# Optimization experiments

Hardware: AMD Instinct MI355X
Metric: run time of the kernel (lower is better)

Reference implementation:

```python
import jax, jax.numpy as jnp
import numpy as np

TOPK = 8
N_EXPERTS = 64
ALPHA = 0.001


def setup_inputs() -> dict:
    key = jax.random.key(0)
    k1, k2 = jax.random.split(key)
    B, S, H = 4, 4096, 4096
    x = jax.random.normal(k1, (B, S, H), dtype=jnp.float32)
    # kaiming-uniform-ish router weight, bound = sqrt(6/((1+5)*H)) = 1/sqrt(H)
    bound = 1.0 / np.sqrt(H)
    weight = jax.random.uniform(k2, (N_EXPERTS, H), dtype=jnp.float32,
                                minval=-bound, maxval=bound)
    return {"x": x, "weight": weight}


def reference(x, weight):
    B, S, H = x.shape
    E = weight.shape[0]
    tokens = x.reshape(-1, H)                      # (T, H), T = B*S
    logits = jnp.einsum('th,eh->te', tokens, weight)  # router GEMM (T, E)
    scores = jax.nn.softmax(logits, axis=-1)
    # top-k selection (torch uses sorted=False; same set of values/indices)
    topk_weight, topk_idx = jax.lax.top_k(scores, TOPK)  # (T, k)
    # normalize top-k probs (norm_topk_prob=True, topk>1)
    topk_weight = topk_weight / (topk_weight.sum(axis=1, keepdims=True) + 1e-20)
    # seq-aux load-balancing loss (training path, alpha > 0, seq_aux=True)
    idx_flat = topk_idx.reshape(B, S * TOPK)                 # (B, S*k)
    ce = jax.nn.one_hot(idx_flat, E, dtype=jnp.float32).sum(axis=1)  # scatter_add of ones
    ce = ce / (S * TOPK / E)                                  # (B, E)
    mean_scores = scores.reshape(B, S, E).mean(axis=1)        # (B, E)
    aux_loss = (ce * mean_scores).sum(axis=1).mean() * ALPHA
    return topk_idx, topk_weight, aux_loss
```

## Files before the change

kernel.cpp:

```cpp
#include <hip/hip_runtime.h>
#include <math.h>

#define H 4096
#define NE 64
#define KTOP 8
#define BT 64
#define TTOT 16384
#define NBLK (TTOT / BT)
#define TAU 1e-4f
#define DELTA 1e-3f

typedef __attribute__((ext_vector_type(8))) short bf16x8;
typedef __attribute__((ext_vector_type(4))) float f32x4;

union U4S8 { uint4 u; bf16x8 s; };

__device__ __forceinline__ unsigned bf16_rne(float f) {
  unsigned b = __float_as_uint(f);
  b += 0x7fffu + ((b >> 16) & 1u);
  return b >> 16;
}

__global__ __launch_bounds__(256) void w_prep(const float* __restrict__ w,
                                              uint4* __restrict__ wsimg) {
  const int sid = blockIdx.x * 256 + threadIdx.x;
  const int e = sid >> 9;
  const int rem = sid & 511;
  const int c = rem >> 2;
  const int s = rem & 3;
  const float* src = w + (size_t)e * H + c * 32 + s * 8;
  float4 f0 = *(const float4*)src;
  float4 f1 = *(const float4*)(src + 4);
  float xf[8] = {f0.x, f0.y, f0.z, f0.w, f1.x, f1.y, f1.z, f1.w};
  unsigned hu[8], lu[8];
#pragma unroll
  for (int j = 0; j < 8; ++j) {
    hu[j] = bf16_rne(xf[j]);
    float hf = __uint_as_float(hu[j] << 16);
    lu[j] = bf16_rne(xf[j] - hf);
  }
  uint4 hp, lp;
  hp.x = hu[0] | (hu[1] << 16); hp.y = hu[2] | (hu[3] << 16);
  hp.z = hu[4] | (hu[5] << 16); hp.w = hu[6] | (hu[7] << 16);
  lp.x = lu[0] | (lu[1] << 16); lp.y = lu[2] | (lu[3] << 16);
  lp.z = lu[4] | (lu[5] << 16); lp.w = lu[6] | (lu[7] << 16);
  const int slotp = s ^ ((e >> 1) & 3);
  wsimg[(size_t)c * 256 + e * 4 + slotp] = hp;
  wsimg[(size_t)128 * 256 + (size_t)c * 256 + e * 4 + slotp] = lp;
}

__device__ __forceinline__ void cvt_split(const float4 a, const float4 b,
                                          bf16x8* hi, bf16x8* lo) {
  float xf[8] = {a.x, a.y, a.z, a.w, b.x, b.y, b.z, b.w};
  unsigned ph[4], pl[4];
#pragma unroll
  for (int q = 0; q < 4; ++q)
    asm("v_cvt_pk_bf16_f32 %0, %1, %2" : "=v"(ph[q])
        : "v"(xf[2 * q]), "v"(xf[2 * q + 1]));
  float rs[8];
#pragma unroll
  for (int q = 0; q < 4; ++q) {
    rs[2 * q]     = xf[2 * q]     - __uint_as_float(ph[q] << 16);
    rs[2 * q + 1] = xf[2 * q + 1] - __uint_as_float(ph[q] & 0xffff0000u);
  }
#pragma unroll
  for (int q = 0; q < 4; ++q)
    asm("v_cvt_pk_bf16_f32 %0, %1, %2" : "=v"(pl[q])
        : "v"(rs[2 * q]), "v"(rs[2 * q + 1]));
  U4S8 h, l;
  h.u = (uint4){ph[0], ph[1], ph[2], ph[3]};
  l.u = (uint4){pl[0], pl[1], pl[2], pl[3]};
  *hi = h.s;
  *lo = l.s;
}

#define GLDS(GP, LP)                                                   \
  __builtin_amdgcn_global_load_lds(                                    \
      (const __attribute__((address_space(1))) void*)(GP),             \
      (__attribute__((address_space(3))) void*)(LP), 16, 0, 0)

__global__ __launch_bounds__(256, 1) void moe_pass1(
    const float* __restrict__ x, const uint4* __restrict__ wsimg,
    float* __restrict__ out, unsigned* __restrict__ wmask,
    float* __restrict__ waux) {
  extern __shared__ __align__(16) char smraw[];
  const int tid = threadIdx.x;
  const int lane = tid & 63;
  const int wid = tid >> 6;
  const int tok0 = blockIdx.x * BT;
  const int trow = lane & 15;
  const int kgrp = lane >> 4;

  const char* xsrc[4];
#pragma unroll
  for (int j = 0; j < 4; ++j) {
    const int Lb = j * 4096 + tid * 16;
    const int row = Lb >> 8;
    const int inrow = Lb & 255;
    const int sin = inrow ^ ((row & 7) << 4);
    xsrc[j] = (const char*)(x + (size_t)(tok0 + row) * H) + sin;
  }
  const uint4* wsrc[4];
#pragma unroll
  for (int j = 0; j < 4; ++j)
    wsrc[j] = wsimg + (size_t)(j >> 1) * (128 * 256) + (j & 1) * 256 + tid;

  f32x4 acc[4];
#pragma unroll
  for (int et = 0; et < 4; ++et) acc[et] = (f32x4){0.f, 0.f, 0.f, 0.f};

#define ISSUE_STEP(KC, BUF)                                             \
  do {                                                                  \
    char* bb = smraw + (BUF) * 32768 + (wid << 10);                     \
    _Pragma("unroll") for (int j = 0; j < 4; ++j)                       \
      GLDS(xsrc[j] + (size_t)(KC) * 256, bb + j * 4096);                \
    _Pragma("unroll") for (int j = 0; j < 4; ++j)                       \
      GLDS((const char*)(wsrc[j] + (size_t)(KC) * 512),                 \
           bb + 16384 + j * 4096);                                      \
  } while (0)

  ISSUE_STEP(0, 0);
  ISSUE_STEP(1, 1);
  ISSUE_STEP(2, 2);

  const int arow = wid * 16 + trow;
  const int sx = (trow & 7) << 4;
  const int abase = arow * 256 + kgrp * 32;
  int entry[4];
#pragma unroll
  for (int et = 0; et < 4; ++et) {
    const int e = et * 16 + trow;
    entry[et] = (e * 4 + (kgrp ^ ((e >> 1) & 3))) * 16;
  }

#pragma unroll 1
  for (int kc = 0; kc < 64; ++kc) {
    if (kc < 62) {
      asm volatile("s_waitcnt vmcnt(16)" ::: "memory");
    } else if (kc == 62) {
      asm volatile("s_waitcnt vmcnt(8)" ::: "memory");
    } else {
      asm volatile("s_waitcnt vmcnt(0)" ::: "memory");
    }
    __builtin_amdgcn_s_barrier();
    asm volatile("" ::: "memory");
    if (kc + 3 < 64) ISSUE_STEP(kc + 3, (kc + 3) & 3);

    const char* bufp = smraw + (kc & 3) * 32768;
#pragma unroll
    for (int sub = 0; sub < 2; ++sub) {
      float4 v0 = *(const float4*)(bufp + ((abase + sub * 128) ^ sx));
      float4 v1 = *(const float4*)(bufp + ((abase + sub * 128 + 16) ^ sx));
      bf16x8 ah, al;
      cvt_split(v0, v1, &ah, &al);
#pragma unroll
      for (int et = 0; et < 4; ++et) {
        U4S8 bh, bl;
        bh.u = *(const uint4*)(bufp + 16384 + sub * 4096 + entry[et]);
        bl.u = *(const uint4*)(bufp + 16384 + (2 + sub) * 4096 + entry[et]);
        acc[et] = __builtin_amdgcn_mfma_f32_16x16x32_bf16(ah, bh.s, acc[et], 0, 0, 0);
        acc[et] = __builtin_amdgcn_mfma_f32_16x16x32_bf16(ah, bl.s, acc[et], 0, 0, 0);
        acc[et] = __builtin_amdgcn_mfma_f32_16x16x32_bf16(al, bh.s, acc[et], 0, 0, 0);
      }
    }
  }

  __syncthreads();
  float* lg = (float*)smraw;
  float* msumA = (float*)(smraw + 16896);
  float* cntA = (float*)(smraw + 17920);
#pragma unroll
  for (int et = 0; et < 4; ++et)
#pragma unroll
    for (int r = 0; r < 4; ++r)
      lg[(wid * 16 + kgrp * 4 + r) * 66 + et * 16 + trow] = acc[et][r];
  __syncthreads();

  float msum = 0.f;
  int cnt = 0;
#pragma unroll 1
  for (int it = 0; it < 16; ++it) {
    const int t = wid * 16 + it;
    const float lf = lg[t * 66 + lane];

    float m = lf;
#pragma unroll
    for (int off = 32; off; off >>= 1) m = fmaxf(m, __shfl_xor(m, off));
    float p = expf(lf - m);
    float s = p;
#pragma unroll
    for (int off = 32; off; off >>= 1) s += __shfl_xor(s, off);
    msum += p / s;

    float cur = lf;
    float myv = 0.f;
    int myi = 0;
#pragma unroll
    for (int r = 0; r < 9; ++r) {
      float v = cur;
      int ix = lane;
#pragma unroll
      for (int off = 1; off < 64; off <<= 1) {
        float ov = __shfl_xor(v, off);
        int oi = __shfl_xor(ix, off);
        if (ov > v || (ov == v && oi < ix)) { v = ov; ix = oi; }
      }
      if (lane == r) { myv = v; myi = ix; }
      if (r < 8 && lane == ix) { cur = -INFINITY; ++cnt; }
    }

    const float m0 = __shfl(myv, 0);
    float e = expf(myv - m0);
    float sv = e;
    sv += __shfl_xor(sv, 1);
    sv += __shfl_xor(sv, 2);
    sv += __shfl_xor(sv, 4);
    const float wgtv = e / sv;
    const int tg = tok0 + t;
    if (lane < KTOP) {
      out[(size_t)tg * KTOP + lane] = (float)myi;
      out[(size_t)TTOT * KTOP + (size_t)tg * KTOP + lane] = wgtv;
    }

    const float nxt = __shfl(myv, (lane + 1) & 63);
    const bool gp = (lane < 8) && (myv - nxt < TAU);
    const unsigned long long anyg = __ballot(gp);
    const float v7 = __shfl(myv, 7);
    const unsigned long long msk = __ballot(lf >= v7 - DELTA);
    if (lane == 0) {
      const unsigned long long mv = anyg ? msk : 0ULL;
      wmask[tg] = (unsigned)mv;
      wmask[TTOT + tg] = (unsigned)(mv >> 32);
    }
  }
  msumA[wid * 64 + lane] = msum;
  cntA[wid * 64 + lane] = (float)cnt;
  __syncthreads();
  if (tid < 64) {
    float c4 = 0.f, m4 = 0.f;
#pragma unroll
    for (int k = 0; k < 4; ++k) {
      c4 += cntA[k * 64 + tid];
      m4 += msumA[k * 64 + tid];
    }
    waux[blockIdx.x * 128 + tid] = c4;
    waux[blockIdx.x * 128 + 64 + tid] = m4;
  }
}

__global__ __launch_bounds__(256) void moe_pass2(
    const float* __restrict__ x, const float* __restrict__ w,
    const unsigned* __restrict__ wmask, float* __restrict__ out) {
  __shared__ unsigned slo[64], shi[64];
  __shared__ double red[4];
  __shared__ double cval[64];
  __shared__ int cidx[64];
  const int tid = threadIdx.x;
  const int lane = tid & 63, wid = tid >> 6;
  const int t0 = blockIdx.x * BT;

  if (tid < 64) { slo[tid] = wmask[t0 + tid]; shi[tid] = wmask[TTOT + t0 + tid]; }
  __syncthreads();
  int myf = (tid < 64) ? ((slo[tid] | shi[tid]) != 0u) : 0;
  if (!__syncthreads_or(myf)) return;

#pragma unroll 1
  for (int tt = 0; tt < BT; ++tt) {
    const unsigned lo = slo[tt], hi = shi[tt];
    if (!(lo | hi)) continue;
    const int t = t0 + tt;
    const unsigned long long m = ((unsigned long long)hi << 32) | lo;
    const float* xr = x + (size_t)t * H;
    int ncand = 0;
#pragma unroll 1
    for (int e = 0; e < 64; ++e) {
      if (!((m >> e) & 1ULL)) continue;
      const float* wr = w + (size_t)e * H;
      double d = 0.0;
#pragma unroll
      for (int q = 0; q < 16; ++q) {
        const int k = tid + 256 * q;
        d = fma((double)xr[k], (double)wr[k], d);
      }
#pragma unroll
      for (int off = 32; off; off >>= 1) d += __shfl_xor(d, off);
      if (lane == 0) red[wid] = d;
      __syncthreads();
      if (tid == 0) {
        cval[ncand] = red[0] + red[1] + red[2] + red[3];
        cidx[ncand] = e;
      }
      __syncthreads();
      ++ncand;
    }
    if (tid == 0) {
      double sel[8];
      int si[8];
      for (int r = 0; r < 8; ++r) {
        int best = 0;
        double bv = -1e300;
        for (int c2 = 0; c2 < ncand; ++c2)
          if (cval[c2] > bv) { bv = cval[c2]; best = c2; }
        sel[r] = cval[best]; si[r] = cidx[best];
        cval[best] = -1e301;
      }
      const double m0 = sel[0];
      float es[8], ssum = 0.f;
      for (int r = 0; r < 8; ++r) { es[r] = expf((float)(sel[r] - m0)); ssum += es[r]; }
      for (int r = 0; r < 8; ++r) {
        out[(size_t)t * KTOP + r] = (float)si[r];
        out[(size_t)TTOT * KTOP + (size_t)t * KTOP + r] = es[r] / ssum;
      }
    }
    __syncthreads();
  }
}

__global__ __launch_bounds__(256) void moe_gate_aux(
    const float* __restrict__ waux, float* __restrict__ out) {
  const int tid = threadIdx.x;
  const int b = tid >> 6, e = tid & 63;
  float cnt = 0.f, ms = 0.f;
#pragma unroll 4
  for (int j = 0; j < 64; ++j) {
    const int blk = b * 64 + j;
    cnt += waux[blk * 128 + e];
    ms += waux[blk * 128 + 64 + e];
  }
  float term = (cnt * (1.f / 512.f)) * (ms * (1.f / 4096.f));
  __shared__ float red[4];
#pragma unroll
  for (int off = 32; off; off >>= 1) term += __shfl_xor(term, off);
  if ((tid & 63) == 0) red[tid >> 6] = term;
  __syncthreads();
  if (tid == 0) {
    float tot = red[0] + red[1] + red[2] + red[3];
    out[(size_t)TTOT * KTOP * 2] = tot * (0.001f / 4.f);
  }
}

extern "C" void kernel_launch(void* const* d_in, const int* in_sizes, int n_in,
                              void* d_out, int out_size, void* d_ws, size_t ws_size,
                              hipStream_t stream) {
  (void)in_sizes; (void)n_in; (void)out_size; (void)ws_size;
  const float* x = (const float*)d_in[0];
  const float* w = (const float*)d_in[1];
  float* out = (float*)d_out;
  uint4* wsimg = (uint4*)d_ws;
  unsigned* wmask = (unsigned*)((char*)d_ws + (1 << 21));
  float* waux = (float*)((char*)d_ws + (1 << 21) + 2 * TTOT * 4);
  (void)hipFuncSetAttribute((const void*)moe_pass1,
                            hipFuncAttributeMaxDynamicSharedMemorySize, 131072);
  w_prep<<<128, 256, 0, stream>>>(w, wsimg);
  moe_pass1<<<NBLK, 256, 131072, stream>>>(x, wsimg, out, wmask, waux);
  moe_pass2<<<NBLK, 256, 0, stream>>>(x, w, wmask, out);
  moe_gate_aux<<<1, 256, 0, stream>>>(waux, out);
}
```

Baseline: 240.2 us.

## Restructure router GEMM pass into single-wave blocks of 32 tokens

The main GEMM kernel changes from 256-thread blocks over 64 tokens with 128KB LDS to 64-thread, single-wavefront blocks over 32 tokens with 48KB LDS. Each wave now computes two 16-token tiles and reuses each loaded weight fragment across both, and the k-chunk is halved to 128 bytes, giving 128 iterations. Workgroup barriers and the cross-wave aux reduction are removed. The aim is more resident blocks per CU and no barrier stalls, at the cost of smaller per-step loads, twice the grid size and twice as many partial aux entries for the final reduction.

```diff
diff --git a/kernel.cpp b/kernel.cpp
--- a/kernel.cpp
+++ b/kernel.cpp
@@ -4,9 +4,11 @@
 #define H 4096
 #define NE 64
 #define KTOP 8
-#define BT 64
 #define TTOT 16384
-#define NBLK (TTOT / BT)
+#define BT1 32
+#define NB1 (TTOT / BT1)
+#define BT2 64
+#define NB2 (TTOT / BT2)
 #define TAU 1e-4f
 #define DELTA 1e-3f
 
@@ -79,53 +81,51 @@
       (const __attribute__((address_space(1))) void*)(GP),             \
       (__attribute__((address_space(3))) void*)(LP), 16, 0, 0)
 
-__global__ __launch_bounds__(256, 1) void moe_pass1(
+__global__ __launch_bounds__(64, 1) void moe_pass1(
     const float* __restrict__ x, const uint4* __restrict__ wsimg,
     float* __restrict__ out, unsigned* __restrict__ wmask,
     float* __restrict__ waux) {
   extern __shared__ __align__(16) char smraw[];
-  const int tid = threadIdx.x;
-  const int lane = tid & 63;
-  const int wid = tid >> 6;
-  const int tok0 = blockIdx.x * BT;
+  const int lane = threadIdx.x;
+  const int tok0 = blockIdx.x * BT1;
   const int trow = lane & 15;
   const int kgrp = lane >> 4;
 
-  const char* xsrc[4];
-#pragma unroll
-  for (int j = 0; j < 4; ++j) {
-    const int Lb = j * 4096 + tid * 16;
-    const int row = Lb >> 8;
-    const int inrow = Lb & 255;
-    const int sin = inrow ^ ((row & 7) << 4);
-    xsrc[j] = (const char*)(x + (size_t)(tok0 + row) * H) + sin;
-  }
-  const uint4* wsrc[4];
-#pragma unroll
-  for (int j = 0; j < 4; ++j)
-    wsrc[j] = wsimg + (size_t)(j >> 1) * (128 * 256) + (j & 1) * 256 + tid;
-
-  f32x4 acc[4];
-#pragma unroll
-  for (int et = 0; et < 4; ++et) acc[et] = (f32x4){0.f, 0.f, 0.f, 0.f};
-
-#define ISSUE_STEP(KC, BUF)                                             \
-  do {                                                                  \
-    char* bb = smraw + (BUF) * 32768 + (wid << 10);                     \
-    _Pragma("unroll") for (int j = 0; j < 4; ++j)                       \
-      GLDS(xsrc[j] + (size_t)(KC) * 256, bb + j * 4096);                \
-    _Pragma("unroll") for (int j = 0; j < 4; ++j)                       \
-      GLDS((const char*)(wsrc[j] + (size_t)(KC) * 512),                 \
-           bb + 16384 + j * 4096);                                      \
+  const char* xsrc[2][2];
+#pragma unroll
+  for (int t = 0; t < 2; ++t)
+#pragma unroll
+    for (int j = 0; j < 2; ++j) {
+      const int row = j * 8 + (lane >> 3);
+      const int inrow = (lane & 7) * 16;
+      const int sin = inrow ^ ((row & 7) << 4);
+      xsrc[t][j] = (const char*)(x + (size_t)(tok0 + t * 16 + row) * H) + sin;
+    }
+  const uint4* wsrcb[2] = {wsimg, wsimg + 128 * 256};
+
+  f32x4 acc[2][4];
+#pragma unroll
+  for (int t = 0; t < 2; ++t)
+#pragma unroll
+    for (int et = 0; et < 4; ++et) acc[t][et] = (f32x4){0.f, 0.f, 0.f, 0.f};
+
+#define ISSUE_STEP(KC, BUF)                                              \
+  do {                                                                   \
+    char* bb = smraw + (size_t)(BUF) * 12288;                            \
+    _Pragma("unroll") for (int t = 0; t < 2; ++t)                        \
+      _Pragma("unroll") for (int j = 0; j < 2; ++j)                      \
+        GLDS(xsrc[t][j] + (size_t)(KC) * 128, bb + t * 2048 + j * 1024); \
+    _Pragma("unroll") for (int j = 0; j < 8; ++j)                        \
+      GLDS((const char*)(wsrcb[j >> 2] + (size_t)(KC) * 256 +            \
+                         (j & 3) * 64 + lane),                           \
+           bb + 4096 + (j >> 2) * 4096 + (j & 3) * 1024);                \
   } while (0)
 
   ISSUE_STEP(0, 0);
   ISSUE_STEP(1, 1);
   ISSUE_STEP(2, 2);
 
-  const int arow = wid * 16 + trow;
   const int sx = (trow & 7) << 4;
-  const int abase = arow * 256 + kgrp * 32;
   int entry[4];
 #pragma unroll
   for (int et = 0; et < 4; ++et) {
@@ -134,54 +134,53 @@
   }
 
 #pragma unroll 1
-  for (int kc = 0; kc < 64; ++kc) {
-    if (kc < 62) {
-      asm volatile("s_waitcnt vmcnt(16)" ::: "memory");
-    } else if (kc == 62) {
-      asm volatile("s_waitcnt vmcnt(8)" ::: "memory");
+  for (int kc = 0; kc < 128; ++kc) {
+    if (kc < 126) {
+      asm volatile("s_waitcnt vmcnt(24)" ::: "memory");
+    } else if (kc == 126) {
+      asm volatile("s_waitcnt vmcnt(12)" ::: "memory");
     } else {
       asm volatile("s_waitcnt vmcnt(0)" ::: "memory");
     }
-    __builtin_amdgcn_s_barrier();
-    asm volatile("" ::: "memory");
-    if (kc + 3 < 64) ISSUE_STEP(kc + 3, (kc + 3) & 3);
-
-    const char* bufp = smraw + (kc & 3) * 32768;
-#pragma unroll
-    for (int sub = 0; sub < 2; ++sub) {
-      float4 v0 = *(const float4*)(bufp + ((abase + sub * 128) ^ sx));
-      float4 v1 = *(const float4*)(bufp + ((abase + sub * 128 + 16) ^ sx));
-      bf16x8 ah, al;
-      cvt_split(v0, v1, &ah, &al);
-#pragma unroll
-      for (int et = 0; et < 4; ++et) {
-        U4S8 bh, bl;
-        bh.u = *(const uint4*)(bufp + 16384 + sub * 4096 + entry[et]);
-        bl.u = *(const uint4*)(bufp + 16384 + (2 + sub) * 4096 + entry[et]);
-        acc[et] = __builtin_amdgcn_mfma_f32_16x16x32_bf16(ah, bh.s, acc[et], 0, 0, 0);
-        acc[et] = __builtin_amdgcn_mfma_f32_16x16x32_bf16(ah, bl.s, acc[et], 0, 0, 0);
-        acc[et] = __builtin_amdgcn_mfma_f32_16x16x32_bf16(al, bh.s, acc[et], 0, 0, 0);
-      }
-    }
-  }
-
-  __syncthreads();
+    if (kc + 3 < 128) ISSUE_STEP(kc + 3, (kc + 3) & 3);
+
+    const char* bufp = smraw + (size_t)(kc & 3) * 12288;
+    bf16x8 ah[2], al[2];
+#pragma unroll
+    for (int t = 0; t < 2; ++t) {
+      const char* ab = bufp + t * 2048 + trow * 128;
+      float4 v0 = *(const float4*)(ab + ((kgrp * 32) ^ sx));
+      float4 v1 = *(const float4*)(ab + ((kgrp * 32 + 16) ^ sx));
+      cvt_split(v0, v1, &ah[t], &al[t]);
+    }
+#pragma unroll
+    for (int et = 0; et < 4; ++et) {
+      U4S8 bh, bl;
+      bh.u = *(const uint4*)(bufp + 4096 + entry[et]);
+      bl.u = *(const uint4*)(bufp + 8192 + entry[et]);
+#pragma unroll
+      for (int t = 0; t < 2; ++t) {
+        acc[t][et] = __builtin_amdgcn_mfma_f32_16x16x32_bf16(ah[t], bh.s, acc[t][et], 0, 0, 0);
+        acc[t][et] = __builtin_amdgcn_mfma_f32_16x16x32_bf16(ah[t], bl.s, acc[t][et], 0, 0, 0);
+        acc[t][et] = __builtin_amdgcn_mfma_f32_16x16x32_bf16(al[t], bh.s, acc[t][et], 0, 0, 0);
+      }
+    }
+  }
+
   float* lg = (float*)smraw;
-  float* msumA = (float*)(smraw + 16896);
-  float* cntA = (float*)(smraw + 17920);
-#pragma unroll
-  for (int et = 0; et < 4; ++et)
-#pragma unroll
-    for (int r = 0; r < 4; ++r)
-      lg[(wid * 16 + kgrp * 4 + r) * 66 + et * 16 + trow] = acc[et][r];
-  __syncthreads();
+#pragma unroll
+  for (int t = 0; t < 2; ++t)
+#pragma unroll
+    for (int et = 0; et < 4; ++et)
+#pragma unroll
+      for (int r = 0; r < 4; ++r)
+        lg[(t * 16 + kgrp * 4 + r) * 66 + et * 16 + trow] = acc[t][et][r];
 
   float msum = 0.f;
   int cnt = 0;
 #pragma unroll 1
-  for (int it = 0; it < 16; ++it) {
-    const int t = wid * 16 + it;
-    const float lf = lg[t * 66 + lane];
+  for (int it = 0; it < 32; ++it) {
+    const float lf = lg[it * 66 + lane];
 
     float m = lf;
 #pragma unroll
@@ -216,7 +215,7 @@
     sv += __shfl_xor(sv, 2);
     sv += __shfl_xor(sv, 4);
     const float wgtv = e / sv;
-    const int tg = tok0 + t;
+    const int tg = tok0 + it;
     if (lane < KTOP) {
       out[(size_t)tg * KTOP + lane] = (float)myi;
       out[(size_t)TTOT * KTOP + (size_t)tg * KTOP + lane] = wgtv;
@@ -233,19 +232,8 @@
       wmask[TTOT + tg] = (unsigned)(mv >> 32);
     }
   }
-  msumA[wid * 64 + lane] = msum;
-  cntA[wid * 64 + lane] = (float)cnt;
-  __syncthreads();
-  if (tid < 64) {
-    float c4 = 0.f, m4 = 0.f;
-#pragma unroll
-    for (int k = 0; k < 4; ++k) {
-      c4 += cntA[k * 64 + tid];
-      m4 += msumA[k * 64 + tid];
-    }
-    waux[blockIdx.x * 128 + tid] = c4;
-    waux[blockIdx.x * 128 + 64 + tid] = m4;
-  }
+  waux[blockIdx.x * 128 + lane] = (float)cnt;
+  waux[blockIdx.x * 128 + 64 + lane] = msum;
 }
 
 __global__ __launch_bounds__(256) void moe_pass2(
@@ -257,7 +245,7 @@
   __shared__ int cidx[64];
   const int tid = threadIdx.x;
   const int lane = tid & 63, wid = tid >> 6;
-  const int t0 = blockIdx.x * BT;
+  const int t0 = blockIdx.x * BT2;
 
   if (tid < 64) { slo[tid] = wmask[t0 + tid]; shi[tid] = wmask[TTOT + t0 + tid]; }
   __syncthreads();
@@ -265,7 +253,7 @@
   if (!__syncthreads_or(myf)) return;
 
 #pragma unroll 1
-  for (int tt = 0; tt < BT; ++tt) {
+  for (int tt = 0; tt < BT2; ++tt) {
     const unsigned lo = slo[tt], hi = shi[tt];
     if (!(lo | hi)) continue;
     const int t = t0 + tt;
@@ -322,8 +310,8 @@
   const int b = tid >> 6, e = tid & 63;
   float cnt = 0.f, ms = 0.f;
 #pragma unroll 4
-  for (int j = 0; j < 64; ++j) {
-    const int blk = b * 64 + j;
+  for (int j = 0; j < 128; ++j) {
+    const int blk = b * 128 + j;
     cnt += waux[blk * 128 + e];
     ms += waux[blk * 128 + 64 + e];
   }
@@ -350,9 +338,9 @@
   unsigned* wmask = (unsigned*)((char*)d_ws + (1 << 21));
   float* waux = (float*)((char*)d_ws + (1 << 21) + 2 * TTOT * 4);
   (void)hipFuncSetAttribute((const void*)moe_pass1,
-                            hipFuncAttributeMaxDynamicSharedMemorySize, 131072);
+                            hipFuncAttributeMaxDynamicSharedMemorySize, 49152);
   w_prep<<<128, 256, 0, stream>>>(w, wsimg);
-  moe_pass1<<<NBLK, 256, 131072, stream>>>(x, wsimg, out, wmask, waux);
-  moe_pass2<<<NBLK, 256, 0, stream>>>(x, w, wmask, out);
+  moe_pass1<<<NB1, 64, 49152, stream>>>(x, wsimg, out, wmask, waux);
+  moe_pass2<<<NB2, 256, 0, stream>>>(x, w, wmask, out);
   moe_gate_aux<<<1, 256, 0, stream>>>(waux, out);
 }
```

Measured after the change: 365.3 us. +52.1%, slower.

## Halve pass1 token tile to 32 with 2 waves and triple-buffered LDS

Applied to the files above, without the earlier changes.

The router GEMM pass now processes 32 tokens per block with 128 threads instead of 64 tokens with 256 threads, doubling the block count. The LDS pipeline shrinks from four 32 KB stages to three 24 KB stages with a prefetch distance of two, and the weight tile loads are redistributed across fewer threads. The intent is to let more blocks be resident and spread load across CUs, cutting per-block LDS so occupancy can rise. In exchange the weight tile is streamed twice as often relative to tokens and each block has a shallower prefetch pipeline; the aux reduction is adjusted to the new block count.

```diff
diff --git a/kernel.cpp b/kernel.cpp
--- a/kernel.cpp
+++ b/kernel.cpp
@@ -4,9 +4,11 @@
 #define H 4096
 #define NE 64
 #define KTOP 8
-#define BT 64
 #define TTOT 16384
-#define NBLK (TTOT / BT)
+#define BT1 32
+#define NB1 (TTOT / BT1)
+#define BT2 64
+#define NB2 (TTOT / BT2)
 #define TAU 1e-4f
 #define DELTA 1e-3f
 
@@ -79,7 +81,7 @@
       (const __attribute__((address_space(1))) void*)(GP),             \
       (__attribute__((address_space(3))) void*)(LP), 16, 0, 0)
 
-__global__ __launch_bounds__(256, 1) void moe_pass1(
+__global__ __launch_bounds__(128, 1) void moe_pass1(
     const float* __restrict__ x, const uint4* __restrict__ wsimg,
     float* __restrict__ out, unsigned* __restrict__ wmask,
     float* __restrict__ waux) {
@@ -87,45 +89,47 @@
   const int tid = threadIdx.x;
   const int lane = tid & 63;
   const int wid = tid >> 6;
-  const int tok0 = blockIdx.x * BT;
+  const int tok0 = blockIdx.x * BT1;
   const int trow = lane & 15;
   const int kgrp = lane >> 4;
 
   const char* xsrc[4];
 #pragma unroll
-  for (int j = 0; j < 4; ++j) {
-    const int Lb = j * 4096 + tid * 16;
-    const int row = Lb >> 8;
-    const int inrow = Lb & 255;
+  for (int q = 0; q < 4; ++q) {
+    const int a = q * 2048 + tid * 16;
+    const int tile = a >> 12;
+    const int row = (a >> 8) & 15;
+    const int inrow = a & 255;
     const int sin = inrow ^ ((row & 7) << 4);
-    xsrc[j] = (const char*)(x + (size_t)(tok0 + row) * H) + sin;
-  }
-  const uint4* wsrc[4];
-#pragma unroll
-  for (int j = 0; j < 4; ++j)
-    wsrc[j] = wsimg + (size_t)(j >> 1) * (128 * 256) + (j & 1) * 256 + tid;
+    xsrc[q] = (const char*)(x + (size_t)(tok0 + tile * 16 + row) * H) + sin;
+  }
+  const uint4* wsrc[8];
+  int wdst[8];
+#pragma unroll
+  for (int j = 0; j < 8; ++j) {
+    const int hilo = j >> 2, sub = (j >> 1) & 1, half = j & 1;
+    wsrc[j] = wsimg + (size_t)hilo * (128 * 256) + sub * 256 + half * 128 + tid;
+    wdst[j] = 8192 + hilo * 8192 + sub * 4096 + half * 2048 + tid * 16;
+  }
 
   f32x4 acc[4];
 #pragma unroll
   for (int et = 0; et < 4; ++et) acc[et] = (f32x4){0.f, 0.f, 0.f, 0.f};
 
-#define ISSUE_STEP(KC, BUF)                                             \
-  do {                                                                  \
-    char* bb = smraw + (BUF) * 32768 + (wid << 10);                     \
-    _Pragma("unroll") for (int j = 0; j < 4; ++j)                       \
-      GLDS(xsrc[j] + (size_t)(KC) * 256, bb + j * 4096);                \
-    _Pragma("unroll") for (int j = 0; j < 4; ++j)                       \
-      GLDS((const char*)(wsrc[j] + (size_t)(KC) * 512),                 \
-           bb + 16384 + j * 4096);                                      \
+#define ISSUE_STEP(KC, BUF)                                              \
+  do {                                                                   \
+    char* bb = smraw + (size_t)(BUF) * 24576;                            \
+    _Pragma("unroll") for (int q = 0; q < 4; ++q)                        \
+      GLDS(xsrc[q] + (size_t)(KC) * 256, bb + q * 2048 + tid * 16);      \
+    _Pragma("unroll") for (int j = 0; j < 8; ++j)                        \
+      GLDS((const char*)(wsrc[j] + (size_t)(KC) * 512), bb + wdst[j]);   \
   } while (0)
 
   ISSUE_STEP(0, 0);
   ISSUE_STEP(1, 1);
-  ISSUE_STEP(2, 2);
-
-  const int arow = wid * 16 + trow;
+
   const int sx = (trow & 7) << 4;
-  const int abase = arow * 256 + kgrp * 32;
+  const int abase = wid * 4096 + trow * 256;
   int entry[4];
 #pragma unroll
   for (int et = 0; et < 4; ++et) {
@@ -135,29 +139,27 @@
 
 #pragma unroll 1
   for (int kc = 0; kc < 64; ++kc) {
-    if (kc < 62) {
-      asm volatile("s_waitcnt vmcnt(16)" ::: "memory");
-    } else if (kc == 62) {
-      asm volatile("s_waitcnt vmcnt(8)" ::: "memory");
+    if (kc < 63) {
+      asm volatile("s_waitcnt vmcnt(12)" ::: "memory");
     } else {
       asm volatile("s_waitcnt vmcnt(0)" ::: "memory");
     }
     __builtin_amdgcn_s_barrier();
     asm volatile("" ::: "memory");
-    if (kc + 3 < 64) ISSUE_STEP(kc + 3, (kc + 3) & 3);
-
-    const char* bufp = smraw + (kc & 3) * 32768;
+    if (kc + 2 < 64) ISSUE_STEP(kc + 2, (kc + 2) % 3);
+
+    const char* bufp = smraw + (size_t)(kc % 3) * 24576;
 #pragma unroll
     for (int sub = 0; sub < 2; ++sub) {
-      float4 v0 = *(const float4*)(bufp + ((abase + sub * 128) ^ sx));
-      float4 v1 = *(const float4*)(bufp + ((abase + sub * 128 + 16) ^ sx));
+      float4 v0 = *(const float4*)(bufp + abase + ((sub * 128 + kgrp * 32) ^ sx));
+      float4 v1 = *(const float4*)(bufp + abase + ((sub * 128 + kgrp * 32 + 16) ^ sx));
       bf16x8 ah, al;
       cvt_split(v0, v1, &ah, &al);
 #pragma unroll
       for (int et = 0; et < 4; ++et) {
         U4S8 bh, bl;
-        bh.u = *(const uint4*)(bufp + 16384 + sub * 4096 + entry[et]);
-        bl.u = *(const uint4*)(bufp + 16384 + (2 + sub) * 4096 + entry[et]);
+        bh.u = *(const uint4*)(bufp + 8192 + sub * 4096 + entry[et]);
+        bl.u = *(const uint4*)(bufp + 16384 + sub * 4096 + entry[et]);
         acc[et] = __builtin_amdgcn_mfma_f32_16x16x32_bf16(ah, bh.s, acc[et], 0, 0, 0);
         acc[et] = __builtin_amdgcn_mfma_f32_16x16x32_bf16(ah, bl.s, acc[et], 0, 0, 0);
         acc[et] = __builtin_amdgcn_mfma_f32_16x16x32_bf16(al, bh.s, acc[et], 0, 0, 0);
@@ -167,8 +169,8 @@
 
   __syncthreads();
   float* lg = (float*)smraw;
-  float* msumA = (float*)(smraw + 16896);
-  float* cntA = (float*)(smraw + 17920);
+  float* msumA = (float*)(smraw + 8448);
+  float* cntA = (float*)(smraw + 8960);
 #pragma unroll
   for (int et = 0; et < 4; ++et)
 #pragma unroll
@@ -237,14 +239,8 @@
   cntA[wid * 64 + lane] = (float)cnt;
   __syncthreads();
   if (tid < 64) {
-    float c4 = 0.f, m4 = 0.f;
-#pragma unroll
-    for (int k = 0; k < 4; ++k) {
-      c4 += cntA[k * 64 + tid];
-      m4 += msumA[k * 64 + tid];
-    }
-    waux[blockIdx.x * 128 + tid] = c4;
-    waux[blockIdx.x * 128 + 64 + tid] = m4;
+    waux[blockIdx.x * 128 + tid] = cntA[tid] + cntA[64 + tid];
+    waux[blockIdx.x * 128 + 64 + tid] = msumA[tid] + msumA[64 + tid];
   }
 }
 
@@ -257,7 +253,7 @@
   __shared__ int cidx[64];
   const int tid = threadIdx.x;
   const int lane = tid & 63, wid = tid >> 6;
-  const int t0 = blockIdx.x * BT;
+  const int t0 = blockIdx.x * BT2;
 
   if (tid < 64) { slo[tid] = wmask[t0 + tid]; shi[tid] = wmask[TTOT + t0 + tid]; }
   __syncthreads();
@@ -265,7 +261,7 @@
   if (!__syncthreads_or(myf)) return;
 
 #pragma unroll 1
-  for (int tt = 0; tt < BT; ++tt) {
+  for (int tt = 0; tt < BT2; ++tt) {
     const unsigned lo = slo[tt], hi = shi[tt];
     if (!(lo | hi)) continue;
     const int t = t0 + tt;
@@ -322,8 +318,8 @@
   const int b = tid >> 6, e = tid & 63;
   float cnt = 0.f, ms = 0.f;
 #pragma unroll 4
-  for (int j = 0; j < 64; ++j) {
-    const int blk = b * 64 + j;
+  for (int j = 0; j < 128; ++j) {
+    const int blk = b * 128 + j;
     cnt += waux[blk * 128 + e];
     ms += waux[blk * 128 + 64 + e];
   }
@@ -350,9 +346,9 @@
   unsigned* wmask = (unsigned*)((char*)d_ws + (1 << 21));
   float* waux = (float*)((char*)d_ws + (1 << 21) + 2 * TTOT * 4);
   (void)hipFuncSetAttribute((const void*)moe_pass1,
-                            hipFuncAttributeMaxDynamicSharedMemorySize, 131072);
+                            hipFuncAttributeMaxDynamicSharedMemorySize, 73728);
   w_prep<<<128, 256, 0, stream>>>(w, wsimg);
-  moe_pass1<<<NBLK, 256, 131072, stream>>>(x, wsimg, out, wmask, waux);
-  moe_pass2<<<NBLK, 256, 0, stream>>>(x, w, wmask, out);
+  moe_pass1<<<NB1, 128, 73728, stream>>>(x, wsimg, out, wmask, waux);
+  moe_pass2<<<NB2, 256, 0, stream>>>(x, w, wmask, out);
   moe_gate_aux<<<1, 256, 0, stream>>>(waux, out);
 }
```

New measurement: 246.7 us. +2.7%, slower.
